# Performance work log

Hardware: AMD Instinct MI355X
Metric: run time of the kernel (lower is better)

## Reference

```python
import jax, jax.numpy as jnp
import numpy as np

H, W = 200, 200
HEADS, LEVELS, POINTS = 8, 1, 4
D = 256
HD = D // HEADS
P = LEVELS * POINTS  # levels folded into points axis (num_levels=1)


def setup_inputs() -> dict:
    key = jax.random.key(0)
    ks = jax.random.split(key, 10)
    B, N = 2, H * W
    s = 1.0 / np.sqrt(D)
    return {
        "x": jax.random.normal(ks[0], (B, N, D), jnp.float32),
        "x_pos": jax.random.normal(ks[1], (B, N, D), jnp.float32) * 0.02,
        "W_off": jax.random.normal(ks[2], (D, HEADS * P * 2), jnp.float32) * 0.01,
        "b_off": jax.random.normal(ks[3], (HEADS * P * 2,), jnp.float32) * 2.0,
        "W_attn": jax.random.normal(ks[4], (D, HEADS * P), jnp.float32) * s,
        "b_attn": jnp.zeros((HEADS * P,), jnp.float32),
        "W_val": jax.random.normal(ks[5], (D, D), jnp.float32) * s,
        "b_val": jnp.zeros((D,), jnp.float32),
        "W_out": jax.random.normal(ks[6], (D, D), jnp.float32) * s,
        "b_out": jnp.zeros((D,), jnp.float32),
    }


def _msda(x, x_pos, W_off, b_off, W_attn, b_attn, W_val, b_val, W_out, b_out):
    B, N, _ = x.shape
    # reference points: pixel centers normalized to [0,1]  -> [N,2] (x,y)
    ry, rx = jnp.meshgrid(jnp.linspace(0.5, H - 0.5, H) / H,
                          jnp.linspace(0.5, W - 0.5, W) / W, indexing="ij")
    ref = jnp.stack([rx.reshape(-1), ry.reshape(-1)], -1).astype(x.dtype)  # [N,2]

    q = x + x_pos  # query_pos added before projections (mmcv behavior)
    off = (q @ W_off + b_off).reshape(B, N, HEADS, P, 2)
    attn = jax.nn.softmax((q @ W_attn + b_attn).reshape(B, N, HEADS, P), axis=-1)
    v = (x @ W_val + b_val).reshape(B, N, HEADS, HD)

    # sampling locations in [0,1], offsets normalized by (W,H)
    loc = ref[None, :, None, None, :] + off / jnp.array([W, H], x.dtype)
    # pixel coords for grid_sample(align_corners=False): p = loc*size - 0.5
    px = (loc[..., 0] * W - 0.5).transpose(0, 2, 1, 3)  # [B,heads,N,P]
    py = (loc[..., 1] * H - 0.5).transpose(0, 2, 1, 3)
    aw = attn.transpose(0, 2, 1, 3)                      # [B,heads,N,P]
    vmap_ = v.transpose(0, 2, 1, 3)                      # [B,heads,N(spatial),HD]

    x0 = jnp.floor(px)
    y0 = jnp.floor(py)
    lx, ly = px - x0, py - y0
    x0i = x0.astype(jnp.int32)
    y0i = y0.astype(jnp.int32)

    out = jnp.zeros((B, HEADS, N, HD), x.dtype)
    corners = [(x0i, y0i, (1 - lx) * (1 - ly)),
               (x0i + 1, y0i, lx * (1 - ly)),
               (x0i, y0i + 1, (1 - lx) * ly),
               (x0i + 1, y0i + 1, lx * ly)]
    for ix, iy, wgt in corners:  # fixed 4-corner bilinear, zero padding
        valid = ((ix >= 0) & (ix < W) & (iy >= 0) & (iy < H)).astype(x.dtype)
        idx = jnp.clip(iy, 0, H - 1) * W + jnp.clip(ix, 0, W - 1)  # [B,heads,N,P]
        g = jnp.take_along_axis(vmap_, idx.reshape(B, HEADS, -1)[..., None], axis=2)
        g = g.reshape(B, HEADS, N, P, HD)
        out = out + jnp.einsum("bhnpd,bhnp->bhnd", g, wgt * valid * aw)

    out = out.transpose(0, 2, 1, 3).reshape(B, N, D)
    out = out @ W_out + b_out
    return x + out  # identity residual (dropout is identity at inference)


def reference(x, x_pos, W_off, b_off, W_attn, b_attn, W_val, b_val, W_out, b_out):
    return _msda(x, x_pos, W_off, b_off, W_attn, b_attn, W_val, b_val, W_out, b_out)
```

## Files before the change

### kernel.cpp

```cpp
#include <hip/hip_runtime.h>

#define H_IMG 200
#define W_IMG 200
#define NTOK  40000
#define ROWS  80000
#define HEADS 8

typedef __attribute__((ext_vector_type(8))) short bf16x8;
typedef __attribute__((ext_vector_type(4))) float f32x4;

__device__ __forceinline__ unsigned short f2bf(float f) {
  unsigned u = __float_as_uint(f);
  u += 0x7fffu + ((u >> 16) & 1u);
  return (unsigned short)(u >> 16);
}
__device__ __forceinline__ float bfl(unsigned u) { return __uint_as_float(u << 16); }
__device__ __forceinline__ float bfh(unsigned u) { return __uint_as_float(u & 0xffff0000u); }

__global__ __launch_bounds__(256) void prep_weights(
    const float* __restrict__ W_val, const float* __restrict__ W_off,
    const float* __restrict__ W_attn, const float* __restrict__ W_out,
    const float* __restrict__ b_off, const float* __restrict__ b_attn,
    unsigned short* __restrict__ Wv_t, unsigned short* __restrict__ Wca_t,
    unsigned short* __restrict__ Wo_t, float* __restrict__ biasc)
{
  int tid = blockIdx.x * 256 + threadIdx.x;
  int n = tid >> 8, k = tid & 255;
  Wv_t[n * 256 + k] = f2bf(W_val[k * 256 + n]);
  Wo_t[n * 256 + k] = f2bf(W_out[k * 256 + n]);
  if (tid < 96 * 256) {
    float w = (n < 64) ? W_off[k * 64 + n] : W_attn[k * 32 + (n - 64)];
    Wca_t[tid] = f2bf(w);
  }
  if (tid < 96) biasc[tid] = (tid < 64) ? b_off[tid] : b_attn[tid - 64];
}

template<int NCHUNK, int NT, int AMODE, int EPI>
__global__ __launch_bounds__(256, 2) void gemm_wide(
    const float* __restrict__ Af0, const float* __restrict__ Af1,
    const unsigned short* __restrict__ Abf,
    const unsigned short* __restrict__ Bt,
    const float* __restrict__ bias, const float* __restrict__ xres,
    float* __restrict__ outf, unsigned short* __restrict__ outb)
{
  __shared__ unsigned short As[64][264];
  __shared__ unsigned short Bs[NT * 16][264];
  const int tid = threadIdx.x;
  const int m0 = blockIdx.x * 64;

  if (AMODE == 2) {
#pragma unroll
    for (int j = 0; j < 8; ++j) {
      int flat = tid + j * 256;
      int row = flat >> 5, seg = flat & 31;
      uint4 u = *(const uint4*)(Abf + (size_t)(m0 + row) * 256 + seg * 8);
      *(uint4*)&As[row][seg * 8] = u;
    }
  } else {
#pragma unroll
    for (int j = 0; j < 16; ++j) {
      int flat = tid + j * 256;
      int row = flat >> 6, seg = flat & 63;
      size_t gi = (size_t)(m0 + row) * 256 + seg * 4;
      float4 a = *(const float4*)(Af0 + gi);
      if (AMODE == 1) {
        float4 b = *(const float4*)(Af1 + gi);
        a.x += b.x; a.y += b.y; a.z += b.z; a.w += b.w;
      }
      unsigned lo = (unsigned)f2bf(a.x) | ((unsigned)f2bf(a.y) << 16);
      unsigned hi = (unsigned)f2bf(a.z) | ((unsigned)f2bf(a.w) << 16);
      *(uint2*)&As[row][seg * 4] = make_uint2(lo, hi);
    }
  }

  const int wave = tid >> 6;
  const int lane = tid & 63;
  const int lr = lane & 15;
  const int lk = lane >> 4;

#pragma unroll
  for (int ch = 0; ch < NCHUNK; ++ch) {
    const int n0 = ch * (NT * 16);
    __syncthreads();
#pragma unroll
    for (int j = 0; j < NT * 2; ++j) {
      int flat = tid + j * 256;
      int row = flat >> 5, seg = flat & 31;
      uint4 u = *(const uint4*)(Bt + (size_t)(n0 + row) * 256 + seg * 8);
      *(uint4*)&Bs[row][seg * 8] = u;
    }
    __syncthreads();

    f32x4 acc[NT];
#pragma unroll
    for (int nt = 0; nt < NT; ++nt) acc[nt] = (f32x4){0.f, 0.f, 0.f, 0.f};
#pragma unroll
    for (int kt = 0; kt < 8; ++kt) {
      bf16x8 af = *(const bf16x8*)&As[wave * 16 + lr][kt * 32 + lk * 8];
#pragma unroll
      for (int nt = 0; nt < NT; ++nt) {
        bf16x8 bfr = *(const bf16x8*)&Bs[nt * 16 + lr][kt * 32 + lk * 8];
        acc[nt] = __builtin_amdgcn_mfma_f32_16x16x32_bf16(af, bfr, acc[nt], 0, 0, 0);
      }
    }

#pragma unroll
    for (int nt = 0; nt < NT; ++nt) {
      const int gcol = n0 + nt * 16 + lr;
      const float bv = bias[gcol];
#pragma unroll
      for (int r = 0; r < 4; ++r) {
        const int grow = m0 + wave * 16 + lk * 4 + r;
        float val = acc[nt][r] + bv;
        if (EPI == 0) {
          outb[(size_t)grow * 256 + gcol] = f2bf(val);
        } else if (EPI == 2) {
          size_t gi = (size_t)grow * 256 + gcol;
          outf[gi] = val + xres[gi];
        } else {
          if (gcol >= 64) {
            float m1 = fmaxf(val, __shfl_xor(val, 1));
            float mx = fmaxf(m1, __shfl_xor(m1, 2));
            float e = __expf(val - mx);
            float s1 = e + __shfl_xor(e, 1);
            float s = s1 + __shfl_xor(s1, 2);
            val = e / s;
          }
          outf[(size_t)grow * 96 + gcol] = val;
        }
      }
    }
  }
}

__global__ __launch_bounds__(256, 4) void sample_k(
    const unsigned short* __restrict__ vbf,
    const float* __restrict__ smp,
    unsigned short* __restrict__ sampled)
{
  const int NB = 2500, q = NB / 8, r = NB % 8;
  int bid = blockIdx.x;
  int xcd = bid & 7, i = bid >> 3;
  int swz = (xcd < r) ? (xcd * (q + 1) + i)
                      : (r * (q + 1) + (xcd - r) * q + i);
  const int tid = swz * 256 + threadIdx.x;
  const int t = tid >> 3;
  const int h = tid & 7;
  const int b = t / NTOK;
  const int n = t - b * NTOK;
  const int ry = n / W_IMG;
  const int cx = n - ry * W_IMG;
  const float* sp = smp + (size_t)t * 96;
  const unsigned short* vb = vbf + (size_t)b * NTOK * 256 + h * 32;

  float acc[32];
#pragma unroll
  for (int i2 = 0; i2 < 32; ++i2) acc[i2] = 0.f;

#pragma unroll
  for (int p = 0; p < 4; ++p) {
    float ox = sp[h * 8 + p * 2 + 0];
    float oy = sp[h * 8 + p * 2 + 1];
    float aw = sp[64 + h * 4 + p];
    float px = (float)cx + ox;
    float py = (float)ry + oy;
    float fx = floorf(px), fy = floorf(py);
    int x0 = (int)fx, y0 = (int)fy;
    float lx = px - fx, ly = py - fy;
    float w00 = (1.f - lx) * (1.f - ly) * aw;
    float w10 = lx * (1.f - ly) * aw;
    float w01 = (1.f - lx) * ly * aw;
    float w11 = lx * ly * aw;
#pragma unroll
    for (int cc = 0; cc < 4; ++cc) {
      int ix = x0 + (cc & 1);
      int iy = y0 + (cc >> 1);
      float w = (cc == 0) ? w00 : (cc == 1) ? w10 : (cc == 2) ? w01 : w11;
      if (ix >= 0 && ix < W_IMG && iy >= 0 && iy < H_IMG) {
        const unsigned short* g = vb + (size_t)(iy * W_IMG + ix) * 256;
#pragma unroll
        for (int q2 = 0; q2 < 4; ++q2) {
          uint4 u = *(const uint4*)(g + q2 * 8);
          acc[q2 * 8 + 0] += w * bfl(u.x); acc[q2 * 8 + 1] += w * bfh(u.x);
          acc[q2 * 8 + 2] += w * bfl(u.y); acc[q2 * 8 + 3] += w * bfh(u.y);
          acc[q2 * 8 + 4] += w * bfl(u.z); acc[q2 * 8 + 5] += w * bfh(u.z);
          acc[q2 * 8 + 6] += w * bfl(u.w); acc[q2 * 8 + 7] += w * bfh(u.w);
        }
      }
    }
  }
  unsigned uo[16];
#pragma unroll
  for (int i2 = 0; i2 < 16; ++i2)
    uo[i2] = (unsigned)f2bf(acc[2 * i2]) | ((unsigned)f2bf(acc[2 * i2 + 1]) << 16);
  uint4* dst = (uint4*)(sampled + (size_t)t * 256 + h * 32);
  dst[0] = make_uint4(uo[0], uo[1], uo[2], uo[3]);
  dst[1] = make_uint4(uo[4], uo[5], uo[6], uo[7]);
  dst[2] = make_uint4(uo[8], uo[9], uo[10], uo[11]);
  dst[3] = make_uint4(uo[12], uo[13], uo[14], uo[15]);
}

extern "C" void kernel_launch(void* const* d_in, const int* in_sizes, int n_in,
                              void* d_out, int out_size, void* d_ws, size_t ws_size,
                              hipStream_t stream) {
  const float* x      = (const float*)d_in[0];
  const float* x_pos  = (const float*)d_in[1];
  const float* W_off  = (const float*)d_in[2];
  const float* b_off  = (const float*)d_in[3];
  const float* W_attn = (const float*)d_in[4];
  const float* b_attn = (const float*)d_in[5];
  const float* W_val  = (const float*)d_in[6];
  const float* b_val  = (const float*)d_in[7];
  const float* W_out  = (const float*)d_in[8];
  const float* b_out  = (const float*)d_in[9];
  float* out = (float*)d_out;

  char* ws = (char*)d_ws;
  unsigned short* Wv_t    = (unsigned short*)(ws);
  unsigned short* Wo_t    = (unsigned short*)(ws + 131072);
  unsigned short* Wca_t   = (unsigned short*)(ws + 262144);
  float*          biasc   = (float*)(ws + 311296);
  unsigned short* vbf     = (unsigned short*)(ws + 311680);
  float*          smp     = (float*)(ws + 41271680);
  unsigned short* sampled = (unsigned short*)(ws + 71991680);

  prep_weights<<<256, 256, 0, stream>>>(W_val, W_off, W_attn, W_out,
                                        b_off, b_attn, Wv_t, Wca_t, Wo_t, biasc);
  gemm_wide<4, 4, 0, 0><<<1250, 256, 0, stream>>>(
      x, nullptr, nullptr, Wv_t, b_val, nullptr, nullptr, vbf);
  gemm_wide<2, 3, 1, 1><<<1250, 256, 0, stream>>>(
      x, x_pos, nullptr, Wca_t, biasc, nullptr, smp, nullptr);
  sample_k<<<2500, 256, 0, stream>>>(vbf, smp, sampled);
  gemm_wide<4, 4, 2, 2><<<1250, 256, 0, stream>>>(
      nullptr, nullptr, sampled, Wo_t, b_out, x, out, nullptr);
}
```

Before: 363.1 us.

## Fuse projections into one kernel and fuse sampling with output GEMM

Merges the value projection and the offset/attention projection into a single kernel that loads x once and reuses the bf16 tile in shared memory, adding x_pos in place. Fuses bilinear sampling with the output projection so sampled features stay in shared memory instead of round-tripping through global memory. Sampling gathers become branchless with clamped addresses and zeroed weights. The fused sampling kernel runs at lower occupancy and its query input is rounded twice to bf16, which changes numerics slightly.

After: 331.4 us. -8.7%, faster.

```diff
diff --git a/kernel.cpp b/kernel.cpp
--- a/kernel.cpp
+++ b/kernel.cpp
@@ -4,7 +4,6 @@
 #define W_IMG 200
 #define NTOK  40000
 #define ROWS  80000
-#define HEADS 8
 
 typedef __attribute__((ext_vector_type(8))) short bf16x8;
 typedef __attribute__((ext_vector_type(4))) float f32x4;
@@ -35,169 +34,250 @@
   if (tid < 96) biasc[tid] = (tid < 64) ? b_off[tid] : b_attn[tid - 64];
 }
 
-template<int NCHUNK, int NT, int AMODE, int EPI>
-__global__ __launch_bounds__(256, 2) void gemm_wide(
-    const float* __restrict__ Af0, const float* __restrict__ Af1,
-    const unsigned short* __restrict__ Abf,
-    const unsigned short* __restrict__ Bt,
-    const float* __restrict__ bias, const float* __restrict__ xres,
-    float* __restrict__ outf, unsigned short* __restrict__ outb)
+__global__ __launch_bounds__(256, 2) void vproj_k(
+    const float* __restrict__ x, const float* __restrict__ x_pos,
+    const unsigned short* __restrict__ Wv_t,
+    const unsigned short* __restrict__ Wca_t,
+    const float* __restrict__ b_val, const float* __restrict__ biasc,
+    unsigned short* __restrict__ vbf, float* __restrict__ smp)
 {
   __shared__ unsigned short As[64][264];
-  __shared__ unsigned short Bs[NT * 16][264];
+  __shared__ unsigned short Bs[64][264];
   const int tid = threadIdx.x;
   const int m0 = blockIdx.x * 64;
-
-  if (AMODE == 2) {
+  const int wave = tid >> 6, lane = tid & 63;
+  const int lr = lane & 15, lk = lane >> 4;
+
+#pragma unroll
+  for (int j = 0; j < 16; ++j) {
+    int flat = tid + j * 256;
+    int row = flat >> 6, seg = flat & 63;
+    float4 a = *(const float4*)(x + (size_t)(m0 + row) * 256 + seg * 4);
+    unsigned lo = (unsigned)f2bf(a.x) | ((unsigned)f2bf(a.y) << 16);
+    unsigned hi = (unsigned)f2bf(a.z) | ((unsigned)f2bf(a.w) << 16);
+    *(uint2*)&As[row][seg * 4] = make_uint2(lo, hi);
+  }
+
+#pragma unroll
+  for (int ch = 0; ch < 4; ++ch) {
+    __syncthreads();
 #pragma unroll
     for (int j = 0; j < 8; ++j) {
       int flat = tid + j * 256;
       int row = flat >> 5, seg = flat & 31;
-      uint4 u = *(const uint4*)(Abf + (size_t)(m0 + row) * 256 + seg * 8);
-      *(uint4*)&As[row][seg * 8] = u;
-    }
-  } else {
-#pragma unroll
-    for (int j = 0; j < 16; ++j) {
-      int flat = tid + j * 256;
-      int row = flat >> 6, seg = flat & 63;
-      size_t gi = (size_t)(m0 + row) * 256 + seg * 4;
-      float4 a = *(const float4*)(Af0 + gi);
-      if (AMODE == 1) {
-        float4 b = *(const float4*)(Af1 + gi);
-        a.x += b.x; a.y += b.y; a.z += b.z; a.w += b.w;
-      }
-      unsigned lo = (unsigned)f2bf(a.x) | ((unsigned)f2bf(a.y) << 16);
-      unsigned hi = (unsigned)f2bf(a.z) | ((unsigned)f2bf(a.w) << 16);
-      *(uint2*)&As[row][seg * 4] = make_uint2(lo, hi);
-    }
-  }
-
-  const int wave = tid >> 6;
-  const int lane = tid & 63;
-  const int lr = lane & 15;
-  const int lk = lane >> 4;
-
-#pragma unroll
-  for (int ch = 0; ch < NCHUNK; ++ch) {
-    const int n0 = ch * (NT * 16);
-    __syncthreads();
-#pragma unroll
-    for (int j = 0; j < NT * 2; ++j) {
+      *(uint4*)&Bs[row][seg * 8] =
+          *(const uint4*)(Wv_t + (size_t)(ch * 64 + row) * 256 + seg * 8);
+    }
+    __syncthreads();
+    f32x4 acc[4];
+#pragma unroll
+    for (int nt = 0; nt < 4; ++nt) acc[nt] = (f32x4){0.f, 0.f, 0.f, 0.f};
+#pragma unroll
+    for (int kt = 0; kt < 8; ++kt) {
+      bf16x8 af = *(const bf16x8*)&As[wave * 16 + lr][kt * 32 + lk * 8];
+#pragma unroll
+      for (int nt = 0; nt < 4; ++nt) {
+        bf16x8 bfr = *(const bf16x8*)&Bs[nt * 16 + lr][kt * 32 + lk * 8];
+        acc[nt] = __builtin_amdgcn_mfma_f32_16x16x32_bf16(af, bfr, acc[nt], 0, 0, 0);
+      }
+    }
+#pragma unroll
+    for (int nt = 0; nt < 4; ++nt) {
+      const int gcol = ch * 64 + nt * 16 + lr;
+      const float bv = b_val[gcol];
+#pragma unroll
+      for (int r = 0; r < 4; ++r) {
+        const int grow = m0 + wave * 16 + lk * 4 + r;
+        vbf[(size_t)grow * 256 + gcol] = f2bf(acc[nt][r] + bv);
+      }
+    }
+  }
+
+  __syncthreads();
+#pragma unroll
+  for (int j = 0; j < 16; ++j) {
+    int flat = tid + j * 256;
+    int row = flat >> 6, seg = flat & 63;
+    float4 p = *(const float4*)(x_pos + (size_t)(m0 + row) * 256 + seg * 4);
+    uint2 cur = *(uint2*)&As[row][seg * 4];
+    float v0 = bfl(cur.x) + p.x, v1 = bfh(cur.x) + p.y;
+    float v2 = bfl(cur.y) + p.z, v3 = bfh(cur.y) + p.w;
+    *(uint2*)&As[row][seg * 4] =
+        make_uint2((unsigned)f2bf(v0) | ((unsigned)f2bf(v1) << 16),
+                   (unsigned)f2bf(v2) | ((unsigned)f2bf(v3) << 16));
+  }
+
+#pragma unroll
+  for (int ch = 0; ch < 2; ++ch) {
+    __syncthreads();
+#pragma unroll
+    for (int j = 0; j < 6; ++j) {
       int flat = tid + j * 256;
       int row = flat >> 5, seg = flat & 31;
-      uint4 u = *(const uint4*)(Bt + (size_t)(n0 + row) * 256 + seg * 8);
-      *(uint4*)&Bs[row][seg * 8] = u;
-    }
-    __syncthreads();
-
-    f32x4 acc[NT];
-#pragma unroll
-    for (int nt = 0; nt < NT; ++nt) acc[nt] = (f32x4){0.f, 0.f, 0.f, 0.f};
+      *(uint4*)&Bs[row][seg * 8] =
+          *(const uint4*)(Wca_t + (size_t)(ch * 48 + row) * 256 + seg * 8);
+    }
+    __syncthreads();
+    f32x4 acc[3];
+#pragma unroll
+    for (int nt = 0; nt < 3; ++nt) acc[nt] = (f32x4){0.f, 0.f, 0.f, 0.f};
 #pragma unroll
     for (int kt = 0; kt < 8; ++kt) {
       bf16x8 af = *(const bf16x8*)&As[wave * 16 + lr][kt * 32 + lk * 8];
 #pragma unroll
-      for (int nt = 0; nt < NT; ++nt) {
+      for (int nt = 0; nt < 3; ++nt) {
         bf16x8 bfr = *(const bf16x8*)&Bs[nt * 16 + lr][kt * 32 + lk * 8];
         acc[nt] = __builtin_amdgcn_mfma_f32_16x16x32_bf16(af, bfr, acc[nt], 0, 0, 0);
       }
     }
-
-#pragma unroll
-    for (int nt = 0; nt < NT; ++nt) {
-      const int gcol = n0 + nt * 16 + lr;
-      const float bv = bias[gcol];
+#pragma unroll
+    for (int nt = 0; nt < 3; ++nt) {
+      const int gcol = ch * 48 + nt * 16 + lr;
+      const float bv = biasc[gcol];
 #pragma unroll
       for (int r = 0; r < 4; ++r) {
         const int grow = m0 + wave * 16 + lk * 4 + r;
         float val = acc[nt][r] + bv;
-        if (EPI == 0) {
-          outb[(size_t)grow * 256 + gcol] = f2bf(val);
-        } else if (EPI == 2) {
-          size_t gi = (size_t)grow * 256 + gcol;
-          outf[gi] = val + xres[gi];
-        } else {
-          if (gcol >= 64) {
-            float m1 = fmaxf(val, __shfl_xor(val, 1));
-            float mx = fmaxf(m1, __shfl_xor(m1, 2));
-            float e = __expf(val - mx);
-            float s1 = e + __shfl_xor(e, 1);
-            float s = s1 + __shfl_xor(s1, 2);
-            val = e / s;
-          }
-          outf[(size_t)grow * 96 + gcol] = val;
+        if (gcol >= 64) {
+          float m1 = fmaxf(val, __shfl_xor(val, 1));
+          float mx = fmaxf(m1, __shfl_xor(m1, 2));
+          float e = __expf(val - mx);
+          float s1 = e + __shfl_xor(e, 1);
+          float s = s1 + __shfl_xor(s1, 2);
+          val = e / s;
         }
-      }
-    }
-  }
-}
-
-__global__ __launch_bounds__(256, 4) void sample_k(
+        smp[(size_t)grow * 96 + gcol] = val;
+      }
+    }
+  }
+}
+
+__global__ __launch_bounds__(256, 2) void sampout_k(
     const unsigned short* __restrict__ vbf,
     const float* __restrict__ smp,
-    unsigned short* __restrict__ sampled)
+    const unsigned short* __restrict__ Wo_t,
+    const float* __restrict__ b_out, const float* __restrict__ x,
+    float* __restrict__ out)
 {
-  const int NB = 2500, q = NB / 8, r = NB % 8;
+  __shared__ unsigned short As[64][264];
+  __shared__ unsigned short Bs[64][264];
+  const int tid = threadIdx.x;
   int bid = blockIdx.x;
-  int xcd = bid & 7, i = bid >> 3;
-  int swz = (xcd < r) ? (xcd * (q + 1) + i)
-                      : (r * (q + 1) + (xcd - r) * q + i);
-  const int tid = swz * 256 + threadIdx.x;
-  const int t = tid >> 3;
-  const int h = tid & 7;
-  const int b = t / NTOK;
-  const int n = t - b * NTOK;
-  const int ry = n / W_IMG;
-  const int cx = n - ry * W_IMG;
-  const float* sp = smp + (size_t)t * 96;
-  const unsigned short* vb = vbf + (size_t)b * NTOK * 256 + h * 32;
-
-  float acc[32];
-#pragma unroll
-  for (int i2 = 0; i2 < 32; ++i2) acc[i2] = 0.f;
-
-#pragma unroll
-  for (int p = 0; p < 4; ++p) {
-    float ox = sp[h * 8 + p * 2 + 0];
-    float oy = sp[h * 8 + p * 2 + 1];
-    float aw = sp[64 + h * 4 + p];
-    float px = (float)cx + ox;
-    float py = (float)ry + oy;
-    float fx = floorf(px), fy = floorf(py);
-    int x0 = (int)fx, y0 = (int)fy;
-    float lx = px - fx, ly = py - fy;
-    float w00 = (1.f - lx) * (1.f - ly) * aw;
-    float w10 = lx * (1.f - ly) * aw;
-    float w01 = (1.f - lx) * ly * aw;
-    float w11 = lx * ly * aw;
-#pragma unroll
-    for (int cc = 0; cc < 4; ++cc) {
-      int ix = x0 + (cc & 1);
-      int iy = y0 + (cc >> 1);
-      float w = (cc == 0) ? w00 : (cc == 1) ? w10 : (cc == 2) ? w01 : w11;
-      if (ix >= 0 && ix < W_IMG && iy >= 0 && iy < H_IMG) {
-        const unsigned short* g = vb + (size_t)(iy * W_IMG + ix) * 256;
-#pragma unroll
-        for (int q2 = 0; q2 < 4; ++q2) {
-          uint4 u = *(const uint4*)(g + q2 * 8);
-          acc[q2 * 8 + 0] += w * bfl(u.x); acc[q2 * 8 + 1] += w * bfh(u.x);
-          acc[q2 * 8 + 2] += w * bfl(u.y); acc[q2 * 8 + 3] += w * bfh(u.y);
-          acc[q2 * 8 + 4] += w * bfl(u.z); acc[q2 * 8 + 5] += w * bfh(u.z);
-          acc[q2 * 8 + 6] += w * bfl(u.w); acc[q2 * 8 + 7] += w * bfh(u.w);
-        }
-      }
-    }
-  }
-  unsigned uo[16];
-#pragma unroll
-  for (int i2 = 0; i2 < 16; ++i2)
-    uo[i2] = (unsigned)f2bf(acc[2 * i2]) | ((unsigned)f2bf(acc[2 * i2 + 1]) << 16);
-  uint4* dst = (uint4*)(sampled + (size_t)t * 256 + h * 32);
-  dst[0] = make_uint4(uo[0], uo[1], uo[2], uo[3]);
-  dst[1] = make_uint4(uo[4], uo[5], uo[6], uo[7]);
-  dst[2] = make_uint4(uo[8], uo[9], uo[10], uo[11]);
-  dst[3] = make_uint4(uo[12], uo[13], uo[14], uo[15]);
+  int xcd = bid & 7, ii = bid >> 3;
+  int swz = (xcd < 2) ? xcd * 157 + ii : 2 * 157 + (xcd - 2) * 156 + ii;
+  const int tok0 = swz * 64;
+
+#pragma unroll
+  for (int pp = 0; pp < 2; ++pp) {
+    const int pair = tid + pp * 256;
+    const int lt = pair >> 3, h = pair & 7;
+    const int t = tok0 + lt;
+    const int b = t / NTOK;
+    const int n = t - b * NTOK;
+    const int ry = n / W_IMG, cx = n - ry * W_IMG;
+    const float* sp = smp + (size_t)t * 96;
+    float4 o01 = *(const float4*)(sp + h * 8);
+    float4 o23 = *(const float4*)(sp + h * 8 + 4);
+    float4 aw4 = *(const float4*)(sp + 64 + h * 4);
+    const unsigned short* vb = vbf + (size_t)b * NTOK * 256 + h * 32;
+
+    float offs[8] = {o01.x, o01.y, o01.z, o01.w, o23.x, o23.y, o23.z, o23.w};
+    float aws[4] = {aw4.x, aw4.y, aw4.z, aw4.w};
+
+    const unsigned short* gp[16];
+    float wv[16];
+#pragma unroll
+    for (int p = 0; p < 4; ++p) {
+      float px = (float)cx + offs[2 * p];
+      float py = (float)ry + offs[2 * p + 1];
+      float fx = floorf(px), fy = floorf(py);
+      int x0 = (int)fx, y0 = (int)fy;
+      float lx = px - fx, ly = py - fy;
+      float cw[4] = {(1.f - lx) * (1.f - ly), lx * (1.f - ly),
+                     (1.f - lx) * ly, lx * ly};
+#pragma unroll
+      for (int cc = 0; cc < 4; ++cc) {
+        int ix = x0 + (cc & 1), iy = y0 + (cc >> 1);
+        int ixc = ix < 0 ? 0 : (ix > W_IMG - 1 ? W_IMG - 1 : ix);
+        int iyc = iy < 0 ? 0 : (iy > H_IMG - 1 ? H_IMG - 1 : iy);
+        float w = cw[cc] * aws[p];
+        gp[p * 4 + cc] = vb + (size_t)(iyc * W_IMG + ixc) * 256;
+        wv[p * 4 + cc] = (ix == ixc && iy == iyc) ? w : 0.f;
+      }
+    }
+    float acc[32];
+#pragma unroll
+    for (int i = 0; i < 32; ++i) acc[i] = 0.f;
+#pragma unroll
+    for (int s = 0; s < 16; ++s) {
+      const uint4* g = (const uint4*)gp[s];
+      float w = wv[s];
+      uint4 u0 = g[0], u1 = g[1], u2 = g[2], u3 = g[3];
+      acc[0]  += w * bfl(u0.x); acc[1]  += w * bfh(u0.x);
+      acc[2]  += w * bfl(u0.y); acc[3]  += w * bfh(u0.y);
+      acc[4]  += w * bfl(u0.z); acc[5]  += w * bfh(u0.z);
+      acc[6]  += w * bfl(u0.w); acc[7]  += w * bfh(u0.w);
+      acc[8]  += w * bfl(u1.x); acc[9]  += w * bfh(u1.x);
+      acc[10] += w * bfl(u1.y); acc[11] += w * bfh(u1.y);
+      acc[12] += w * bfl(u1.z); acc[13] += w * bfh(u1.z);
+      acc[14] += w * bfl(u1.w); acc[15] += w * bfh(u1.w);
+      acc[16] += w * bfl(u2.x); acc[17] += w * bfh(u2.x);
+      acc[18] += w * bfl(u2.y); acc[19] += w * bfh(u2.y);
+      acc[20] += w * bfl(u2.z); acc[21] += w * bfh(u2.z);
+      acc[22] += w * bfl(u2.w); acc[23] += w * bfh(u2.w);
+      acc[24] += w * bfl(u3.x); acc[25] += w * bfh(u3.x);
+      acc[26] += w * bfl(u3.y); acc[27] += w * bfh(u3.y);
+      acc[28] += w * bfl(u3.z); acc[29] += w * bfh(u3.z);
+      acc[30] += w * bfl(u3.w); acc[31] += w * bfh(u3.w);
+    }
+    unsigned uo[16];
+#pragma unroll
+    for (int i = 0; i < 16; ++i)
+      uo[i] = (unsigned)f2bf(acc[2 * i]) | ((unsigned)f2bf(acc[2 * i + 1]) << 16);
+    uint4* dst = (uint4*)&As[lt][h * 32];
+    dst[0] = make_uint4(uo[0], uo[1], uo[2], uo[3]);
+    dst[1] = make_uint4(uo[4], uo[5], uo[6], uo[7]);
+    dst[2] = make_uint4(uo[8], uo[9], uo[10], uo[11]);
+    dst[3] = make_uint4(uo[12], uo[13], uo[14], uo[15]);
+  }
+
+  const int wave = tid >> 6, lane = tid & 63;
+  const int lr = lane & 15, lk = lane >> 4;
+#pragma unroll
+  for (int ch = 0; ch < 4; ++ch) {
+    if (ch) __syncthreads();
+#pragma unroll
+    for (int j = 0; j < 8; ++j) {
+      int flat = tid + j * 256;
+      int row = flat >> 5, seg = flat & 31;
+      *(uint4*)&Bs[row][seg * 8] =
+          *(const uint4*)(Wo_t + (size_t)(ch * 64 + row) * 256 + seg * 8);
+    }
+    __syncthreads();
+    f32x4 acc[4];
+#pragma unroll
+    for (int nt = 0; nt < 4; ++nt) acc[nt] = (f32x4){0.f, 0.f, 0.f, 0.f};
+#pragma unroll
+    for (int kt = 0; kt < 8; ++kt) {
+      bf16x8 af = *(const bf16x8*)&As[wave * 16 + lr][kt * 32 + lk * 8];
+#pragma unroll
+      for (int nt = 0; nt < 4; ++nt) {
+        bf16x8 bfr = *(const bf16x8*)&Bs[nt * 16 + lr][kt * 32 + lk * 8];
+        acc[nt] = __builtin_amdgcn_mfma_f32_16x16x32_bf16(af, bfr, acc[nt], 0, 0, 0);
+      }
+    }
+#pragma unroll
+    for (int nt = 0; nt < 4; ++nt) {
+      const int gcol = ch * 64 + nt * 16 + lr;
+      const float bv = b_out[gcol];
+#pragma unroll
+      for (int r = 0; r < 4; ++r) {
+        const int grow = tok0 + wave * 16 + lk * 4 + r;
+        size_t gi = (size_t)grow * 256 + gcol;
+        out[gi] = acc[nt][r] + bv + x[gi];
+      }
+    }
+  }
 }
 
 extern "C" void kernel_launch(void* const* d_in, const int* in_sizes, int n_in,
@@ -216,21 +296,16 @@
   float* out = (float*)d_out;
 
   char* ws = (char*)d_ws;
-  unsigned short* Wv_t    = (unsigned short*)(ws);
-  unsigned short* Wo_t    = (unsigned short*)(ws + 131072);
-  unsigned short* Wca_t   = (unsigned short*)(ws + 262144);
-  float*          biasc   = (float*)(ws + 311296);
-  unsigned short* vbf     = (unsigned short*)(ws + 311680);
-  float*          smp     = (float*)(ws + 41271680);
-  unsigned short* sampled = (unsigned short*)(ws + 71991680);
+  unsigned short* Wv_t  = (unsigned short*)(ws);
+  unsigned short* Wo_t  = (unsigned short*)(ws + 131072);
+  unsigned short* Wca_t = (unsigned short*)(ws + 262144);
+  float*          biasc = (float*)(ws + 311296);
+  unsigned short* vbf   = (unsigned short*)(ws + 311680);
+  float*          smp   = (float*)(ws + 41271680);
 
   prep_weights<<<256, 256, 0, stream>>>(W_val, W_off, W_attn, W_out,
                                         b_off, b_attn, Wv_t, Wca_t, Wo_t, biasc);
-  gemm_wide<4, 4, 0, 0><<<1250, 256, 0, stream>>>(
-      x, nullptr, nullptr, Wv_t, b_val, nullptr, nullptr, vbf);
-  gemm_wide<2, 3, 1, 1><<<1250, 256, 0, stream>>>(
-      x, x_pos, nullptr, Wca_t, biasc, nullptr, smp, nullptr);
-  sample_k<<<2500, 256, 0, stream>>>(vbf, smp, sampled);
-  gemm_wide<4, 4, 2, 2><<<1250, 256, 0, stream>>>(
-      nullptr, nullptr, sampled, Wo_t, b_out, x, out, nullptr);
-}
+  vproj_k<<<1250, 256, 0, stream>>>(x, x_pos, Wv_t, Wca_t, b_val, biasc,
+                                    vbf, smp);
+  sampout_k<<<1250, 256, 0, stream>>>(vbf, smp, Wo_t, b_out, x, out);
+}
```
